# Performance work log

Measured on AMD Instinct MI355X. Metric: run time of the kernel, lower is better.

## Reference

```python
import jax, jax.numpy as jnp
import numpy as np

D = 64          # cfg.D_PAIR
NT = 6          # cfg.N_TORSION_OUT
LN_EPS = 1e-5


def _layernorm(x, g, b):
    # torch LayerNorm computed in float32 then cast back
    x32 = x.astype(jnp.float32)
    m = jnp.mean(x32, axis=-1, keepdims=True)
    v = jnp.var(x32, axis=-1, keepdims=True)
    y = (x32 - m) / jnp.sqrt(v + LN_EPS) * g + b
    return y.astype(x.dtype)


def setup_inputs() -> dict:
    key = jax.random.key(0)
    ks = jax.random.split(key, 16)
    B, L = 2, 512
    s = 0.125  # ~xavier scale for fan 64
    inp = {
        "pair": jax.random.normal(ks[0], (B, L, L, D), jnp.float32),
        "torsion": jax.random.normal(ks[1], (B, L, NT), jnp.float32),
        "ln_g": jnp.ones((D,), jnp.float32),
        "ln_b": jnp.zeros((D,), jnp.float32),
        "Wl": jax.random.normal(ks[2], (D, D), jnp.float32) * s,
        "Wr": jax.random.normal(ks[3], (D, D), jnp.float32) * s,
        "Wlg": jax.random.normal(ks[4], (D, D), jnp.float32) * s,
        "blg": jnp.zeros((D,), jnp.float32),
        "Wrg": jax.random.normal(ks[5], (D, D), jnp.float32) * s,
        "brg": jnp.zeros((D,), jnp.float32),
        "Wog": jax.random.normal(ks[6], (D, D), jnp.float32) * s,
        "bog": jnp.zeros((D,), jnp.float32),
        "Wout": jax.random.normal(ks[7], (D, D), jnp.float32) * s,  # 'final' init is zeros; randomized to exercise math
        "bout": jnp.zeros((D,), jnp.float32),
        "lno_g": jnp.ones((D,), jnp.float32),
        "lno_b": jnp.zeros((D,), jnp.float32),
        "Wt": jax.random.normal(ks[8], (1, NT), jnp.float32) * 0.4,
        "bt": jnp.zeros((1,), jnp.float32),
    }
    return inp


def reference(pair, torsion, ln_g, ln_b, Wl, Wr, Wlg, blg, Wrg, brg,
              Wog, bog, Wout, bout, lno_g, lno_b, Wt, bt):
    B, L, _, d = pair.shape
    z = _layernorm(pair, ln_g, ln_b)                         # [B,L,L,D]
    a = (z @ Wl.T) * jax.nn.sigmoid(z @ Wlg.T + blg)         # left proj * gate
    b = (z @ Wr.T) * jax.nn.sigmoid(z @ Wrg.T + brg)         # right proj * gate
    t_w = jax.nn.sigmoid(torsion @ Wt.T + bt)[..., 0]        # [B,L]
    # outgoing=True branch: tw unsqueezed to [B,1,L,1] then transposed(1,2) -> [B,L,1,1]
    a_w = a * t_w[:, :, None, None]
    x = jnp.einsum('bikd,bjkd->bijd', a_w, b) / (L ** 0.5 + 1e-8)
    g = jax.nn.sigmoid(z @ Wog.T + bog)
    out = (_layernorm(x, lno_g, lno_b) @ Wout.T + bout) * g
    return pair + out
```

## Files before the change

kernel.cpp:

```cpp
#include <hip/hip_runtime.h>
#include <stdint.h>

#define LL 512
#define DD 64

typedef __attribute__((ext_vector_type(8))) short bf16x8;
typedef __attribute__((ext_vector_type(4))) float f32x4;

#define MFMA16(a, b, c) __builtin_amdgcn_mfma_f32_16x16x32_bf16((a), (b), (c), 0, 0, 0)

__device__ __forceinline__ float bf2f(unsigned short u) {
    union { unsigned int i; float f; } v; v.i = ((unsigned int)u) << 16; return v.f;
}
__device__ __forceinline__ unsigned short f2bf(float f) {
    union { float f; unsigned int i; } v; v.f = f;
    unsigned int i = v.i;
    return (unsigned short)((i + 0x7FFFu + ((i >> 16) & 1u)) >> 16);
}
__device__ __forceinline__ float sigm(float x) {
    float d = 1.0f + __expf(-x);
    float y = __builtin_amdgcn_rcpf(d);
    return y * __builtin_fmaf(-d, y, 2.0f);
}

__global__ void prep_w(const float* __restrict__ Wl, const float* __restrict__ Wr,
                       const float* __restrict__ Wlg, const float* __restrict__ Wrg,
                       const float* __restrict__ Wog, const float* __restrict__ Wout,
                       unsigned short* __restrict__ Wcat, unsigned short* __restrict__ WoutB) {
    int t = threadIdx.x + blockIdx.x * blockDim.x;
    int stride = blockDim.x * gridDim.x;
    for (int idx = t; idx < 320 * 64; idx += stride) {
        int row = idx >> 6, col = idx & 63;
        int sec = row >> 6, r = row & 63;
        float v;
        switch (sec) {
            case 0:  v = Wl[r * 64 + col];  break;
            case 1:  v = Wlg[r * 64 + col]; break;
            case 2:  v = Wr[r * 64 + col];  break;
            case 3:  v = Wrg[r * 64 + col]; break;
            default: v = Wog[r * 64 + col]; break;
        }
        Wcat[idx] = f2bf(v);
    }
    for (int idx = t; idx < 64 * 64; idx += stride) WoutB[idx] = f2bf(Wout[idx]);
}

__launch_bounds__(256)
__global__ void k1_proj(const float* __restrict__ pair, const float* __restrict__ torsion,
                        const float* __restrict__ ln_g, const float* __restrict__ ln_b,
                        const float* __restrict__ blg, const float* __restrict__ brg,
                        const float* __restrict__ bog, const float* __restrict__ Wt,
                        const float* __restrict__ bt, const unsigned short* __restrict__ Wcat,
                        unsigned short* __restrict__ At, unsigned short* __restrict__ Bt,
                        unsigned short* __restrict__ G) {
    const int bb = blockIdx.z, irow = blockIdx.y, c0 = blockIdx.x * 128;
    const int t = threadIdx.x, w = t >> 6, lane = t & 63;
    const int rsel = lane & 15, koff = lane >> 4;
    const int col = w * 16 + rsel;
    __shared__ unsigned short zs[128][72];
    __shared__ unsigned short awL[64][132];
    __shared__ unsigned short bL[64][132];

    float tww;
    {
        float acc = bt[0];
        #pragma unroll
        for (int n = 0; n < 6; ++n) acc += torsion[(bb * LL + irow) * 6 + n] * Wt[n];
        tww = sigm(acc);
    }

    bf16x8 wfr[5][2];
    #pragma unroll
    for (int s = 0; s < 5; ++s)
        #pragma unroll
        for (int kh = 0; kh < 2; ++kh)
            wfr[s][kh] = *(const bf16x8*)&Wcat[(size_t)(s * 64 + col) * 64 + kh * 32 + koff * 8];
    const float vblg = blg[col], vbrg = brg[col], vbog = bog[col];

    {
        const int sub = lane & 3, rr = lane >> 2;
        const float4* pr4 = (const float4*)(pair + ((size_t)(bb * LL + irow) * LL + c0) * DD);
        #pragma unroll
        for (int p = 0; p < 2; ++p) {
            const int row = w * 32 + p * 16 + rr;
            float4 x[4];
            #pragma unroll
            for (int q = 0; q < 4; ++q) x[q] = pr4[row * 16 + sub * 4 + q];
            float s = 0.f, s2 = 0.f;
            #pragma unroll
            for (int q = 0; q < 4; ++q) {
                s += x[q].x + x[q].y + x[q].z + x[q].w;
                s2 += x[q].x * x[q].x + x[q].y * x[q].y + x[q].z * x[q].z + x[q].w * x[q].w;
            }
            s += __shfl_xor(s, 1);  s2 += __shfl_xor(s2, 1);
            s += __shfl_xor(s, 2);  s2 += __shfl_xor(s2, 2);
            float m = s * 0.015625f;
            float var = s2 * 0.015625f - m * m;
            float rstd = rsqrtf(var + 1e-5f);
            #pragma unroll
            for (int q = 0; q < 4; ++q) {
                float4 lg4 = ((const float4*)ln_g)[sub * 4 + q];
                float4 lb4 = ((const float4*)ln_b)[sub * 4 + q];
                ushort4 zw;
                zw.x = f2bf((x[q].x - m) * rstd * lg4.x + lb4.x);
                zw.y = f2bf((x[q].y - m) * rstd * lg4.y + lb4.y);
                zw.z = f2bf((x[q].z - m) * rstd * lg4.z + lb4.z);
                zw.w = f2bf((x[q].w - m) * rstd * lg4.w + lb4.w);
                *(ushort4*)&zs[row][sub * 16 + q * 4] = zw;
            }
        }
    }
    __syncthreads();

    ushort4 gk[8];
    #pragma unroll
    for (int mi = 0; mi < 8; ++mi) {
        bf16x8 a0 = *(const bf16x8*)&zs[mi * 16 + rsel][koff * 8];
        bf16x8 a1 = *(const bf16x8*)&zs[mi * 16 + rsel][32 + koff * 8];
        f32x4 pl = {0.f, 0.f, 0.f, 0.f}, plg = pl, pr = pl, prg = pl, pog = pl;
        pl  = MFMA16(a0, wfr[0][0], pl);  pl  = MFMA16(a1, wfr[0][1], pl);
        plg = MFMA16(a0, wfr[1][0], plg); plg = MFMA16(a1, wfr[1][1], plg);
        pr  = MFMA16(a0, wfr[2][0], pr);  pr  = MFMA16(a1, wfr[2][1], pr);
        prg = MFMA16(a0, wfr[3][0], prg); prg = MFMA16(a1, wfr[3][1], prg);
        pog = MFMA16(a0, wfr[4][0], pog); pog = MFMA16(a1, wfr[4][1], pog);

        const int crow = mi * 16 + koff * 4;
        unsigned short aw4[4], bm4[4], g4[4];
        #pragma unroll
        for (int r = 0; r < 4; ++r) {
            float av = pl[r] * sigm(plg[r] + vblg) * tww;
            float bv = pr[r] * sigm(prg[r] + vbrg);
            float gv = sigm(pog[r] + vbog);
            aw4[r] = f2bf(av); bm4[r] = f2bf(bv); g4[r] = f2bf(gv);
        }
        *(ushort4*)&awL[col][crow] = make_ushort4(aw4[0], aw4[1], aw4[2], aw4[3]);
        *(ushort4*)&bL[col][crow]  = make_ushort4(bm4[0], bm4[1], bm4[2], bm4[3]);
        gk[mi] = make_ushort4(g4[0], g4[1], g4[2], g4[3]);
    }
    __syncthreads();

    #pragma unroll
    for (int mi = 0; mi < 8; ++mi) {
        const int rbase = mi * 16 + koff * 4;
        zs[rbase + 0][col] = gk[mi].x;
        zs[rbase + 1][col] = gk[mi].y;
        zs[rbase + 2][col] = gk[mi].z;
        zs[rbase + 3][col] = gk[mi].w;
    }
    __syncthreads();

    #pragma unroll
    for (int it = 0; it < 8; ++it) {
        int d = it * 8 + (t >> 5);
        int c8 = (t & 31) * 4;
        size_t base = ((size_t)(bb * 64 + d) * LL + irow) * LL + c0 + c8;
        *(ushort4*)&At[base] = *(const ushort4*)&awL[d][c8];
        *(ushort4*)&Bt[base] = *(const ushort4*)&bL[d][c8];
    }
    #pragma unroll
    for (int it = 0; it < 8; ++it) {
        int r = it * 16 + (t >> 4), cc = (t & 15) * 4;
        size_t pos = (size_t)(bb * LL + irow) * LL + c0 + r;
        *(ushort4*)&G[pos * DD + cc] = *(const ushort4*)&zs[r][cc];
    }
}

__launch_bounds__(256)
__global__ void k2_gemm(const unsigned short* __restrict__ At,
                        const unsigned short* __restrict__ Bt,
                        unsigned short* __restrict__ Xt) {
    int lin = blockIdx.x + (blockIdx.y << 4);
    int nlin = (lin & 7) * 256 + (lin >> 3);
    const int p = nlin >> 4;
    const int tile = nlin & 15;
    const int i0 = (tile >> 2) * 128, j0 = (tile & 3) * 128;
    const unsigned short* Ap = At + (size_t)p * LL * LL + (size_t)i0 * LL;
    const unsigned short* Bp = Bt + (size_t)p * LL * LL + (size_t)j0 * LL;
    __shared__ unsigned short As[128][40], Bs[128][40];
    __shared__ unsigned short Cs[128][136];
    const int t = threadIdx.x, lane = t & 63, w = t >> 6;
    const int rsel = lane & 15, koff = lane >> 4;
    const int wm = w >> 1, wn = w & 1;

    f32x4 acc[4][4];
    #pragma unroll
    for (int i = 0; i < 4; ++i)
        #pragma unroll
        for (int j = 0; j < 4; ++j) acc[i][j] = (f32x4){0.f, 0.f, 0.f, 0.f};

    const int srow0 = t >> 2, skq = t & 3;
    uint4 ra[2], rb[2];
    #pragma unroll
    for (int q = 0; q < 2; ++q) {
        int row = srow0 + q * 64;
        ra[q] = *(const uint4*)&Ap[(size_t)row * LL + skq * 8];
        rb[q] = *(const uint4*)&Bp[(size_t)row * LL + skq * 8];
    }
    for (int k0 = 0; k0 < LL; k0 += 32) {
        #pragma unroll
        for (int q = 0; q < 2; ++q) {
            int row = srow0 + q * 64;
            *(uint4*)&As[row][skq * 8] = ra[q];
            *(uint4*)&Bs[row][skq * 8] = rb[q];
        }
        __syncthreads();
        if (k0 + 32 < LL) {
            #pragma unroll
            for (int q = 0; q < 2; ++q) {
                int row = srow0 + q * 64;
                ra[q] = *(const uint4*)&Ap[(size_t)row * LL + (k0 + 32) + skq * 8];
                rb[q] = *(const uint4*)&Bp[(size_t)row * LL + (k0 + 32) + skq * 8];
            }
        }
        bf16x8 af[4], bfr[4];
        #pragma unroll
        for (int mi = 0; mi < 4; ++mi)
            af[mi] = *(const bf16x8*)&As[wm * 64 + mi * 16 + rsel][koff * 8];
        #pragma unroll
        for (int ni = 0; ni < 4; ++ni)
            bfr[ni] = *(const bf16x8*)&Bs[wn * 64 + ni * 16 + rsel][koff * 8];
        #pragma unroll
        for (int mi = 0; mi < 4; ++mi)
            #pragma unroll
            for (int ni = 0; ni < 4; ++ni)
                acc[mi][ni] = MFMA16(af[mi], bfr[ni], acc[mi][ni]);
        __syncthreads();
    }
    const float s = 1.0f / (sqrtf((float)LL) + 1e-8f);
    #pragma unroll
    for (int mi = 0; mi < 4; ++mi)
        #pragma unroll
        for (int ni = 0; ni < 4; ++ni)
            #pragma unroll
            for (int r = 0; r < 4; ++r)
                Cs[wm * 64 + mi * 16 + koff * 4 + r][wn * 64 + ni * 16 + rsel] =
                    f2bf(acc[mi][ni][r] * s);
    __syncthreads();
    #pragma unroll
    for (int it = 0; it < 8; ++it) {
        int row = it * 16 + (t >> 4), colc = (t & 15) * 8;
        uint4 v = *(const uint4*)&Cs[row][colc];
        *(uint4*)&Xt[((size_t)p * LL + i0 + row) * LL + j0 + colc] = v;
    }
}

__launch_bounds__(256)
__global__ void k3_out(const unsigned short* __restrict__ Xt, const unsigned short* __restrict__ G,
                       const float* __restrict__ pairIn, const unsigned short* __restrict__ WoutB,
                       const float* __restrict__ lno_g, const float* __restrict__ lno_b,
                       const float* __restrict__ bout, float* __restrict__ out) {
    const int bb = blockIdx.z, irow = blockIdx.y, c0 = blockIdx.x * 128;
    const int t = threadIdx.x, w = t >> 6, lane = t & 63;
    __shared__ unsigned short x1[64][128];
    __shared__ unsigned short x2[128][72];

    #pragma unroll
    for (int q = 0; q < 4; ++q) {
        int idx = t + q * 256, d = idx >> 4, c8 = idx & 15;
        uint4 v = *(const uint4*)&Xt[((size_t)(bb * 64 + d) * LL + irow) * LL + c0 + c8 * 8];
        *(uint4*)&x1[d][c8 * 8] = v;
    }
    __syncthreads();
    {
        const int c = t & 127, half = t >> 7;
        unsigned short tmp[32];
        #pragma unroll
        for (int dd = 0; dd < 32; ++dd) tmp[dd] = x1[half * 32 + dd][c];
        #pragma unroll
        for (int q = 0; q < 4; ++q)
            *(uint4*)&x2[c][half * 32 + q * 8] = *(const uint4*)&tmp[q * 8];
    }
    __syncthreads();

    {
        const int sub = lane & 3, rr = lane >> 2;
        #pragma unroll
        for (int p = 0; p < 2; ++p) {
            const int row = w * 32 + p * 16 + rr;
            ushort4 raw[4];
            #pragma unroll
            for (int q = 0; q < 4; ++q) raw[q] = *(const ushort4*)&x2[row][sub * 16 + q * 4];
            float xv[16];
            #pragma unroll
            for (int q = 0; q < 4; ++q) {
                xv[q * 4 + 0] = bf2f(raw[q].x);
                xv[q * 4 + 1] = bf2f(raw[q].y);
                xv[q * 4 + 2] = bf2f(raw[q].z);
                xv[q * 4 + 3] = bf2f(raw[q].w);
            }
            float s = 0.f, s2 = 0.f;
            #pragma unroll
            for (int e = 0; e < 16; ++e) { s += xv[e]; s2 += xv[e] * xv[e]; }
            s += __shfl_xor(s, 1);  s2 += __shfl_xor(s2, 1);
            s += __shfl_xor(s, 2);  s2 += __shfl_xor(s2, 2);
            float m = s * 0.015625f;
            float var = s2 * 0.015625f - m * m;
            float rstd = rsqrtf(var + 1e-5f);
            #pragma unroll
            for (int q = 0; q < 4; ++q) {
                float4 lg4 = ((const float4*)lno_g)[sub * 4 + q];
                float4 lb4 = ((const float4*)lno_b)[sub * 4 + q];
                ushort4 zw;
                zw.x = f2bf((xv[q * 4 + 0] - m) * rstd * lg4.x + lb4.x);
                zw.y = f2bf((xv[q * 4 + 1] - m) * rstd * lg4.y + lb4.y);
                zw.z = f2bf((xv[q * 4 + 2] - m) * rstd * lg4.z + lb4.z);
                zw.w = f2bf((xv[q * 4 + 3] - m) * rstd * lg4.w + lb4.w);
                *(ushort4*)&x2[row][sub * 16 + q * 4] = zw;
            }
        }
    }
    __syncthreads();

    unsigned short* o_lds = &x1[0][0];
    const int rsel = lane & 15, koff = lane >> 4;
    #pragma unroll
    for (int mh = 0; mh < 2; ++mh) {
        const int mi = 2 * w + mh;
        bf16x8 a0 = *(const bf16x8*)&x2[mi * 16 + rsel][koff * 8];
        bf16x8 a1 = *(const bf16x8*)&x2[mi * 16 + rsel][32 + koff * 8];
        #pragma unroll
        for (int n = 0; n < 4; ++n) {
            f32x4 pacc = {0.f, 0.f, 0.f, 0.f};
            const unsigned short* wrow = WoutB + (size_t)(n * 16 + rsel) * 64;
            pacc = MFMA16(a0, *(const bf16x8*)&wrow[koff * 8], pacc);
            pacc = MFMA16(a1, *(const bf16x8*)&wrow[32 + koff * 8], pacc);
            const float bo = bout[n * 16 + rsel];
            #pragma unroll
            for (int r = 0; r < 4; ++r)
                o_lds[(mi * 16 + koff * 4 + r) * 64 + n * 16 + rsel] = f2bf(pacc[r] + bo);
        }
    }
    __syncthreads();

    #pragma unroll
    for (int q = 0; q < 4; ++q) {
        int e = q * 2048 + t * 8;
        int c = e >> 6, o = e & 63;
        size_t pos = (size_t)(bb * LL + irow) * LL + c0 + c;
        uint4 ov = *(const uint4*)&o_lds[c * 64 + o];
        uint4 gv = *(const uint4*)&G[pos * DD + o];
        const unsigned short* ovp = (const unsigned short*)&ov;
        const unsigned short* gvp = (const unsigned short*)&gv;
        float4 p0 = *(const float4*)&pairIn[pos * DD + o];
        float4 p1 = *(const float4*)&pairIn[pos * DD + o + 4];
        float4 r0, r1;
        r0.x = p0.x + bf2f(ovp[0]) * bf2f(gvp[0]);
        r0.y = p0.y + bf2f(ovp[1]) * bf2f(gvp[1]);
        r0.z = p0.z + bf2f(ovp[2]) * bf2f(gvp[2]);
        r0.w = p0.w + bf2f(ovp[3]) * bf2f(gvp[3]);
        r1.x = p1.x + bf2f(ovp[4]) * bf2f(gvp[4]);
        r1.y = p1.y + bf2f(ovp[5]) * bf2f(gvp[5]);
        r1.z = p1.z + bf2f(ovp[6]) * bf2f(gvp[6]);
        r1.w = p1.w + bf2f(ovp[7]) * bf2f(gvp[7]);
        *(float4*)&out[pos * DD + o] = r0;
        *(float4*)&out[pos * DD + o + 4] = r1;
    }
}

extern "C" void kernel_launch(void* const* d_in, const int* in_sizes, int n_in,
                              void* d_out, int out_size, void* d_ws, size_t ws_size,
                              hipStream_t stream) {
    const float* pair    = (const float*)d_in[0];
    const float* torsion = (const float*)d_in[1];
    const float* ln_g    = (const float*)d_in[2];
    const float* ln_b    = (const float*)d_in[3];
    const float* Wl      = (const float*)d_in[4];
    const float* Wr      = (const float*)d_in[5];
    const float* Wlg     = (const float*)d_in[6];
    const float* blg     = (const float*)d_in[7];
    const float* Wrg     = (const float*)d_in[8];
    const float* brg     = (const float*)d_in[9];
    const float* Wog     = (const float*)d_in[10];
    const float* bog     = (const float*)d_in[11];
    const float* Wout    = (const float*)d_in[12];
    const float* bout    = (const float*)d_in[13];
    const float* lno_g   = (const float*)d_in[14];
    const float* lno_b   = (const float*)d_in[15];
    const float* Wt      = (const float*)d_in[16];
    const float* bt      = (const float*)d_in[17];
    float* outp = (float*)d_out;

    const size_t PLANE_B = (size_t)128 * LL * LL * 2;
    const size_t need = 4 * PLANE_B + (320 * 64 + 64 * 64) * 2;
    if (ws_size < need) return;

    char* ws = (char*)d_ws;
    unsigned short* At    = (unsigned short*)(ws);
    unsigned short* Bt_   = (unsigned short*)(ws + PLANE_B);
    unsigned short* G     = (unsigned short*)(ws + 2 * PLANE_B);
    unsigned short* Xt    = (unsigned short*)(ws + 3 * PLANE_B);
    unsigned short* Wcat  = (unsigned short*)(ws + 4 * PLANE_B);
    unsigned short* WoutB = Wcat + 320 * 64;

    prep_w<<<dim3(40), dim3(256), 0, stream>>>(Wl, Wr, Wlg, Wrg, Wog, Wout, Wcat, WoutB);
    k1_proj<<<dim3(4, LL, 2), dim3(256), 0, stream>>>(pair, torsion, ln_g, ln_b, blg, brg,
                                                      bog, Wt, bt, Wcat, At, Bt_, G);
    k2_gemm<<<dim3(16, 128), dim3(256), 0, stream>>>(At, Bt_, Xt);
    k3_out<<<dim3(4, LL, 2), dim3(256), 0, stream>>>(Xt, G, pair, WoutB, lno_g, lno_b, bout, outp);
}
```

Before: 283.6 us.

## Double-buffer k2 GEMM LDS tiles in fragment-native layout with union shared memory

Rewrites the k2 batched GEMM main loop to use two LDS buffers, so the next K-slab is written while the current one is consumed, cutting the two barriers per iteration to one. Each wave's global loads now map directly to the MFMA fragment order, so the LDS reads are contiguous and free of bank conflicts, with no padded rows. The staging buffers and the output tile share one union, and launch bounds now request 4 blocks per CU to raise occupancy. The cost is extra register pressure from the occupancy hint and a more involved indexing scheme.

```diff
diff --git a/kernel.cpp b/kernel.cpp
--- a/kernel.cpp
+++ b/kernel.cpp
@@ -165,7 +165,12 @@
     }
 }
 
-__launch_bounds__(256)
+union K2Sh {
+    unsigned short ab[4][4096];
+    unsigned short cs[128][136];
+};
+
+__launch_bounds__(256, 4)
 __global__ void k2_gemm(const unsigned short* __restrict__ At,
                         const unsigned short* __restrict__ Bt,
                         unsigned short* __restrict__ Xt) {
@@ -176,10 +181,8 @@
     const int i0 = (tile >> 2) * 128, j0 = (tile & 3) * 128;
     const unsigned short* Ap = At + (size_t)p * LL * LL + (size_t)i0 * LL;
     const unsigned short* Bp = Bt + (size_t)p * LL * LL + (size_t)j0 * LL;
-    __shared__ unsigned short As[128][40], Bs[128][40];
-    __shared__ unsigned short Cs[128][136];
+    __shared__ K2Sh sh;
     const int t = threadIdx.x, lane = t & 63, w = t >> 6;
-    const int rsel = lane & 15, koff = lane >> 4;
     const int wm = w >> 1, wn = w & 1;
 
     f32x4 acc[4][4];
@@ -188,44 +191,68 @@
         #pragma unroll
         for (int j = 0; j < 4; ++j) acc[i][j] = (f32x4){0.f, 0.f, 0.f, 0.f};
 
-    const int srow0 = t >> 2, skq = t & 3;
+    const unsigned short* apq[2];
+    const unsigned short* bpq[2];
+    #pragma unroll
+    for (int q = 0; q < 2; ++q) {
+        const int s = w + 4 * q;
+        const int grow = s * 16 + (lane & 15);
+        const int gcol = (lane >> 4) * 8;
+        apq[q] = Ap + (size_t)grow * LL + gcol;
+        bpq[q] = Bp + (size_t)grow * LL + gcol;
+    }
+    const int wofs = w * 512 + lane * 8;
+
     uint4 ra[2], rb[2];
     #pragma unroll
     for (int q = 0; q < 2; ++q) {
-        int row = srow0 + q * 64;
-        ra[q] = *(const uint4*)&Ap[(size_t)row * LL + skq * 8];
-        rb[q] = *(const uint4*)&Bp[(size_t)row * LL + skq * 8];
-    }
-    for (int k0 = 0; k0 < LL; k0 += 32) {
-        #pragma unroll
-        for (int q = 0; q < 2; ++q) {
-            int row = srow0 + q * 64;
-            *(uint4*)&As[row][skq * 8] = ra[q];
-            *(uint4*)&Bs[row][skq * 8] = rb[q];
-        }
-        __syncthreads();
-        if (k0 + 32 < LL) {
+        ra[q] = *(const uint4*)apq[q];
+        rb[q] = *(const uint4*)bpq[q];
+    }
+    #pragma unroll
+    for (int q = 0; q < 2; ++q) {
+        *(uint4*)&sh.ab[0][wofs + q * 2048] = ra[q];
+        *(uint4*)&sh.ab[1][wofs + q * 2048] = rb[q];
+    }
+    __syncthreads();
+
+    for (int k = 0; k < 16; ++k) {
+        const int cur = k & 1;
+        if (k < 15) {
             #pragma unroll
             for (int q = 0; q < 2; ++q) {
-                int row = srow0 + q * 64;
-                ra[q] = *(const uint4*)&Ap[(size_t)row * LL + (k0 + 32) + skq * 8];
-                rb[q] = *(const uint4*)&Bp[(size_t)row * LL + (k0 + 32) + skq * 8];
-            }
-        }
+                apq[q] += 32; bpq[q] += 32;
+                ra[q] = *(const uint4*)apq[q];
+                rb[q] = *(const uint4*)bpq[q];
+            }
+        }
+        const unsigned short* As = sh.ab[cur * 2];
+        const unsigned short* Bs = sh.ab[cur * 2 + 1];
         bf16x8 af[4], bfr[4];
         #pragma unroll
         for (int mi = 0; mi < 4; ++mi)
-            af[mi] = *(const bf16x8*)&As[wm * 64 + mi * 16 + rsel][koff * 8];
+            af[mi] = *(const bf16x8*)&As[(wm * 4 + mi) * 512 + lane * 8];
         #pragma unroll
         for (int ni = 0; ni < 4; ++ni)
-            bfr[ni] = *(const bf16x8*)&Bs[wn * 64 + ni * 16 + rsel][koff * 8];
+            bfr[ni] = *(const bf16x8*)&Bs[(wn * 4 + ni) * 512 + lane * 8];
         #pragma unroll
         for (int mi = 0; mi < 4; ++mi)
             #pragma unroll
             for (int ni = 0; ni < 4; ++ni)
                 acc[mi][ni] = MFMA16(af[mi], bfr[ni], acc[mi][ni]);
+        if (k < 15) {
+            unsigned short* An = sh.ab[(cur ^ 1) * 2];
+            unsigned short* Bn = sh.ab[(cur ^ 1) * 2 + 1];
+            #pragma unroll
+            for (int q = 0; q < 2; ++q) {
+                *(uint4*)&An[wofs + q * 2048] = ra[q];
+                *(uint4*)&Bn[wofs + q * 2048] = rb[q];
+            }
+        }
         __syncthreads();
     }
+
+    const int rsel = lane & 15, koff = lane >> 4;
     const float s = 1.0f / (sqrtf((float)LL) + 1e-8f);
     #pragma unroll
     for (int mi = 0; mi < 4; ++mi)
@@ -233,13 +260,13 @@
         for (int ni = 0; ni < 4; ++ni)
             #pragma unroll
             for (int r = 0; r < 4; ++r)
-                Cs[wm * 64 + mi * 16 + koff * 4 + r][wn * 64 + ni * 16 + rsel] =
+                sh.cs[wm * 64 + mi * 16 + koff * 4 + r][wn * 64 + ni * 16 + rsel] =
                     f2bf(acc[mi][ni][r] * s);
     __syncthreads();
     #pragma unroll
     for (int it = 0; it < 8; ++it) {
         int row = it * 16 + (t >> 4), colc = (t & 15) * 8;
-        uint4 v = *(const uint4*)&Cs[row][colc];
+        uint4 v = *(const uint4*)&sh.cs[row][colc];
         *(uint4*)&Xt[((size_t)p * LL + i0 + row) * LL + j0 + colc] = v;
     }
 }
```

New measurement: 261.0 us. 8.0% less time.

## Load GEMM MFMA fragments directly from global memory, dropping LDS staging

Applied to the files above, without the earlier changes.

The batched GEMM kernel no longer stages A/B tiles through shared memory with register double-buffering and barriers. Each wave now loads its bf16x8 MFMA fragments straight from global memory, relying on L2/L1 for reuse across waves. Launch bounds also request two blocks per SM. This removes the LDS traffic and the two __syncthreads per k-step, at the cost of more global loads with less coalescing, duplicated fetches across waves, and no software prefetch to hide latency.

```diff
diff --git a/kernel.cpp b/kernel.cpp
--- a/kernel.cpp
+++ b/kernel.cpp
@@ -165,7 +165,7 @@
     }
 }
 
-__launch_bounds__(256)
+__launch_bounds__(256, 2)
 __global__ void k2_gemm(const unsigned short* __restrict__ At,
                         const unsigned short* __restrict__ Bt,
                         unsigned short* __restrict__ Xt) {
@@ -174,13 +174,10 @@
     const int p = nlin >> 4;
     const int tile = nlin & 15;
     const int i0 = (tile >> 2) * 128, j0 = (tile & 3) * 128;
-    const unsigned short* Ap = At + (size_t)p * LL * LL + (size_t)i0 * LL;
-    const unsigned short* Bp = Bt + (size_t)p * LL * LL + (size_t)j0 * LL;
-    __shared__ unsigned short As[128][40], Bs[128][40];
+    const int t = threadIdx.x, lane = t & 63, w = t >> 6;
+    const int wm = w >> 1, wn = w & 1;
+    const int rsel = lane & 15, koff = lane >> 4;
     __shared__ unsigned short Cs[128][136];
-    const int t = threadIdx.x, lane = t & 63, w = t >> 6;
-    const int rsel = lane & 15, koff = lane >> 4;
-    const int wm = w >> 1, wn = w & 1;
 
     f32x4 acc[4][4];
     #pragma unroll
@@ -188,44 +185,26 @@
         #pragma unroll
         for (int j = 0; j < 4; ++j) acc[i][j] = (f32x4){0.f, 0.f, 0.f, 0.f};
 
-    const int srow0 = t >> 2, skq = t & 3;
-    uint4 ra[2], rb[2];
-    #pragma unroll
-    for (int q = 0; q < 2; ++q) {
-        int row = srow0 + q * 64;
-        ra[q] = *(const uint4*)&Ap[(size_t)row * LL + skq * 8];
-        rb[q] = *(const uint4*)&Bp[(size_t)row * LL + skq * 8];
-    }
+    const unsigned short* ap =
+        At + (size_t)p * LL * LL + (size_t)(i0 + wm * 64 + rsel) * LL + koff * 8;
+    const unsigned short* bp =
+        Bt + (size_t)p * LL * LL + (size_t)(j0 + wn * 64 + rsel) * LL + koff * 8;
+
     for (int k0 = 0; k0 < LL; k0 += 32) {
-        #pragma unroll
-        for (int q = 0; q < 2; ++q) {
-            int row = srow0 + q * 64;
-            *(uint4*)&As[row][skq * 8] = ra[q];
-            *(uint4*)&Bs[row][skq * 8] = rb[q];
-        }
-        __syncthreads();
-        if (k0 + 32 < LL) {
-            #pragma unroll
-            for (int q = 0; q < 2; ++q) {
-                int row = srow0 + q * 64;
-                ra[q] = *(const uint4*)&Ap[(size_t)row * LL + (k0 + 32) + skq * 8];
-                rb[q] = *(const uint4*)&Bp[(size_t)row * LL + (k0 + 32) + skq * 8];
-            }
-        }
         bf16x8 af[4], bfr[4];
         #pragma unroll
         for (int mi = 0; mi < 4; ++mi)
-            af[mi] = *(const bf16x8*)&As[wm * 64 + mi * 16 + rsel][koff * 8];
+            af[mi] = *(const bf16x8*)(ap + (size_t)mi * 16 * LL + k0);
         #pragma unroll
         for (int ni = 0; ni < 4; ++ni)
-            bfr[ni] = *(const bf16x8*)&Bs[wn * 64 + ni * 16 + rsel][koff * 8];
+            bfr[ni] = *(const bf16x8*)(bp + (size_t)ni * 16 * LL + k0);
         #pragma unroll
         for (int mi = 0; mi < 4; ++mi)
             #pragma unroll
             for (int ni = 0; ni < 4; ++ni)
                 acc[mi][ni] = MFMA16(af[mi], bfr[ni], acc[mi][ni]);
-        __syncthreads();
-    }
+    }
+
     const float s = 1.0f / (sqrtf((float)LL) + 1e-8f);
     #pragma unroll
     for (int mi = 0; mi < 4; ++mi)
```

After: 297.6 us. 4.9% more time.
